# Performance work log

Measured on AMD Instinct MI355X. Metric: run time of the kernel, lower is better.

Reference implementation:

```python
import jax, jax.numpy as jnp
import numpy as np

N_GRAPHS = 1000
P = 300                 # nodes per ring graph
N = N_GRAPHS * P        # 300000 nodes
IN_DIM = 2
HID = 128
OUT_DIM = 2


def _ring_edges():
    idx = jnp.arange(N)
    g = idx // P
    pos = idx % P
    nxt = g * P + (pos + 1) % P
    src = jnp.concatenate([idx, nxt])
    dst = jnp.concatenate([nxt, idx])
    return jnp.stack([src, dst]), g


def setup_inputs() -> dict:
    key = jax.random.key(0)
    ks = jax.random.split(key, 11)
    edge_index, batch = _ring_edges()
    x = jax.random.normal(ks[0], (N, IN_DIM), jnp.float32)

    def glorot(k, fan_in, fan_out):
        lim = np.sqrt(6.0 / (fan_in + fan_out)).astype(np.float32)
        return jax.random.uniform(k, (fan_in, fan_out), jnp.float32, -lim, lim)

    return {
        "x": x,
        "edge_index": edge_index,
        "batch": batch,
        "W1": glorot(ks[1], IN_DIM, HID), "b1": jnp.zeros((HID,), jnp.float32),
        "W2": glorot(ks[2], HID, HID),    "b2": jnp.zeros((HID,), jnp.float32),
        "W3": glorot(ks[3], HID, HID),    "b3": jnp.zeros((HID,), jnp.float32),
        "fw1": glorot(ks[4], HID, HID),   "fb1": jnp.zeros((HID,), jnp.float32),
        "fw2": glorot(ks[5], HID, OUT_DIM), "fb2": jnp.zeros((OUT_DIM,), jnp.float32),
    }


def _gcn_conv(x, W, b, src, dst, norm):
    h = x @ W                              # [N, out]
    msg = h[src] * norm[:, None]           # gather + per-edge scale
    agg = jax.ops.segment_sum(msg, dst, num_segments=N)  # scatter-add
    return agg + b


def reference(x, edge_index, batch, W1, b1, W2, b2, W3, b3, fw1, fb1, fw2, fb2):
    loop = jnp.arange(N)
    src = jnp.concatenate([edge_index[0], loop])
    dst = jnp.concatenate([edge_index[1], loop])
    deg = jax.ops.segment_sum(jnp.ones_like(dst, jnp.float32), dst, num_segments=N)
    dis = jax.lax.rsqrt(deg)               # deg >= 1 due to self-loops
    norm = dis[src] * dis[dst]             # per-edge normalization

    h = jax.nn.relu(_gcn_conv(x, W1, b1, src, dst, norm))
    h = jax.nn.relu(_gcn_conv(h, W2, b2, src, dst, norm))
    h = jax.nn.relu(_gcn_conv(h, W3, b3, src, dst, norm))

    # global mean pool per graph
    sums = jax.ops.segment_sum(h, batch, num_segments=N_GRAPHS)
    cnts = jax.ops.segment_sum(jnp.ones((N,), jnp.float32), batch, num_segments=N_GRAPHS)
    pooled = sums / cnts[:, None]

    out = jax.nn.relu(pooled @ fw1 + fb1)
    out = out @ fw2 + fb2
    return out
```

## Files before the change

### kernel.cpp

```cpp
#include <hip/hip_runtime.h>
#include <hip/hip_bf16.h>
#include <stdint.h>

#define P    300
#define HID  128
#define NG   1000
#define NTL  19

typedef __attribute__((ext_vector_type(8))) short bf16x8;
typedef __attribute__((ext_vector_type(4))) short bf16x4;
typedef __attribute__((ext_vector_type(4))) float f32x4;

__device__ short g_wsw[2 * HID * HID];

__device__ __forceinline__ short f2bf(float f) {
    union { float f; uint32_t u; } v; v.f = f;
    uint32_t r = v.u + 0x7fffu + ((v.u >> 16) & 1u);
    return (short)(r >> 16);
}
__device__ __forceinline__ float bf2f(short s) {
    union { uint32_t u; float f; } v; v.u = ((uint32_t)(uint16_t)s) << 16;
    return v.f;
}
__device__ __forceinline__ uint32_t pkbf2(float a, float b) {
    union { __hip_bfloat162 h; uint32_t u; } cv;
    cv.h = __float22bfloat162_rn(float2{a, b});
    return cv.u;
}
__device__ __forceinline__ float unpk(int v, int ft) {
    return bf2f((short)(ft ? (((uint32_t)v) >> 16) : (v & 0xffff)));
}

__device__ __forceinline__ f32x4 mfma16(bf16x4 a, bf16x4 b, f32x4 c) {
#if __has_builtin(__builtin_amdgcn_mfma_f32_16x16x16bf16_1k)
    return __builtin_amdgcn_mfma_f32_16x16x16bf16_1k(a, b, c, 0, 0, 0);
#else
    asm("v_mfma_f32_16x16x16_bf16 %0, %1, %2, %0" : "+v"(c) : "v"(a), "v"(b));
    return c;
#endif
}

__global__ __launch_bounds__(256) void k_prep(const float* __restrict__ W2,
                                              const float* __restrict__ W3) {
    int b = blockIdx.x;
    const bool perm = (b < 8);
    const float* W = perm ? W2 : W3;
    short* dst = g_wsw + (perm ? 0 : HID * HID);
    int t    = (b & 7) * 256 + threadIdx.x;
    int fkey = t >> 4;
    int kc   = t & 15;
    int fsrc;
    if (perm) {
        int u = fkey >> 5, ft = (fkey >> 4) & 1, l = fkey & 15;
        fsrc = u * 32 + 2 * l + ft;
    } else fsrc = fkey;
    bf16x8 o;
    #pragma unroll
    for (int j = 0; j < 8; ++j)
        o[j] = f2bf(W[(kc * 8 + j) * HID + fsrc]);
    *(bf16x8*)&dst[(fkey * 16 + (kc ^ (fkey & 15))) * 8] = o;
}

template<int POOL>
__device__ __forceinline__ void run_pass(short* __restrict__ buf,
                                         const short* __restrict__ wbase,
                                         const float* __restrict__ bias,
                                         float* __restrict__ pool, int tid) {
    const int lane = tid & 63, wv = tid >> 6;
    const int grp = wv >> 2, w4 = wv & 3;
    const int q = lane >> 4, lm = lane & 15;
    const int ftg0 = w4 * 2;
    bf16x8 wf[2][4];
    #pragma unroll
    for (int ft = 0; ft < 2; ++ft) {
        int fkey = (ftg0 + ft) * 16 + lm;
        #pragma unroll
        for (int kk = 0; kk < 4; ++kk)
            wf[ft][kk] = *(const bf16x8*)&wbase[(fkey * 16 + ((4 * kk + q) ^ lm)) * 8];
    }
    float biaf[2];
    #pragma unroll
    for (int ft = 0; ft < 2; ++ft)
        biaf[ft] = POOL ? bias[(ftg0 + ft) * 16 + lm] : bias[w4 * 32 + 2 * lm + ft];
    const int fpair = w4 * 32 + 2 * lm;
    const int kcs = fpair >> 3, offs = fpair & 7;

    const short ONE = (short)0x3F80;
    bf16x4 Sb = {0, 0, 0, 0}, Sp = {0, 0, 0, 0}, Sn = {0, 0, 0, 0};
    #pragma unroll
    for (int j = 0; j < 4; ++j) {
        const int k = 4 * q + j;
        if (((lm & 3) == 0 && k == lm - 1) || ((lm & 3) == 3 && k == lm + 1))
            Sb[j] = ONE;
        if (lm == 0  && k == 15) Sp[j] = ONE;
        if (lm == 15 && k == 0 ) Sn[j] = ONE;
    }

    float psum[2] = {0.f, 0.f};
    float z[2];

    auto mfma_tile = [&](int t, f32x4 (&G)[2]) {
        const short* tb = buf + t * 2048;
        G[0] = f32x4{0.f, 0.f, 0.f, 0.f};
        G[1] = f32x4{0.f, 0.f, 0.f, 0.f};
        #pragma unroll
        for (int kk = 0; kk < 4; ++kk) {
            bf16x8 af = *(const bf16x8*)&tb[(lm * 16 + ((4 * kk + q) ^ lm)) * 8];
            G[0] = __builtin_amdgcn_mfma_f32_16x16x32_bf16(af, wf[0][kk], G[0], 0, 0, 0);
            G[1] = __builtin_amdgcn_mfma_f32_16x16x32_bf16(af, wf[1][kk], G[1], 0, 0, 0);
        }
    };
    auto pack = [&](const f32x4 (&G)[2], bf16x4 (&d)[2]) {
        #pragma unroll
        for (int ft = 0; ft < 2; ++ft) {
            union { bf16x4 v; uint32_t u[2]; } pk;
            pk.u[0] = pkbf2(G[ft][0], G[ft][1]);
            pk.u[1] = pkbf2(G[ft][2], G[ft][3]);
            d[ft] = pk.v;
        }
    };
    auto store_rows = [&](int T, float (&o)[2][4]) {
        #pragma unroll
        for (int i = 0; i < 4; ++i) {
            int node = T * 16 + q * 4 + i;
            *(uint32_t*)&buf[(node * 16 + (kcs ^ (node & 15))) * 8 + offs] =
                pkbf2(o[0][i], o[1][i]);
        }
    };
    auto accum = [&](float (&o)[2][4]) {
        #pragma unroll
        for (int ft = 0; ft < 2; ++ft)
            psum[ft] += o[ft][0] + o[ft][1] + o[ft][2] + o[ft][3];
    };

    auto epi = [&](const f32x4 (&E)[2], const bf16x4 (&bT)[2],
                   const bf16x4 (&bP)[2], const bf16x4 (&bN)[2],
                   int mode, float (&o)[2][4]) {
        #pragma unroll
        for (int ft = 0; ft < 2; ++ft) {
            f32x4 C = {0.f, 0.f, 0.f, 0.f};
            C = mfma16(Sb, bT[ft], C);
            if (mode != 1) C = mfma16(Sp, bP[ft], C);
            if (mode != 2) C = mfma16(Sn, bN[ft], C);
            const float s0 = E[ft][0] + E[ft][1];
            const float s2 = E[ft][2] + E[ft][3];
            float t0 = C[0] + s0;
            float t1 = s0 + E[ft][2];
            float t2 = E[ft][1] + s2;
            float t3 = s2 + C[3];
            if (mode == 1) t0 += (q == 0) ? z[ft] : 0.f;
            if (mode == 2) t3 += (q == 2) ? z[ft] : 0.f;
            float v0 = fmaf(t0, 1.f / 3.f, biaf[ft]);
            float v1 = fmaf(t1, 1.f / 3.f, biaf[ft]);
            float v2 = fmaf(t2, 1.f / 3.f, biaf[ft]);
            float v3 = fmaf(t3, 1.f / 3.f, biaf[ft]);
            o[ft][0] = v0 > 0.f ? v0 : 0.f;
            o[ft][1] = v1 > 0.f ? v1 : 0.f;
            o[ft][2] = v2 > 0.f ? v2 : 0.f;
            o[ft][3] = v3 > 0.f ? v3 : 0.f;
        }
    };

    const int base = grp ? 10 : 0;
    f32x4 Gh[2];
    bf16x4 bqM[2], bqH[2], bq9p[2];

    {
        f32x4 T[2];
        if (grp == 0) {
            mfma_tile(18, T);
            int v = __shfl((int)pkbf2(T[0][3], T[1][3]), 32 + lm, 64);
            z[0] = unpk(v, 0); z[1] = unpk(v, 1);
            mfma_tile(9, T); pack(T, bq9p);
            Gh[0] = T[0]; Gh[1] = T[1];
            bqM[0] = bq9p[0]; bqM[1] = bq9p[1];
            bqH[0] = bq9p[0]; bqH[1] = bq9p[1];
        } else {
            mfma_tile(0, T);
            int v = __shfl((int)pkbf2(T[0][0], T[1][0]), lm, 64);
            z[0] = unpk(v, 0); z[1] = unpk(v, 1);
            mfma_tile(8, T); pack(T, bqM);
            mfma_tile(9, Gh); pack(Gh, bqH);
            bq9p[0] = bqM[0]; bq9p[1] = bqM[1];
        }
    }

    for (int j = 1; j <= 5; ++j) {
        f32x4 Gc[2], Gd[2];
        bf16x4 bqC[2], bqD[2];
        if (j < 5) {
            int t0r = base + 2 * j - 2;
            mfma_tile(t0r,     Gc); pack(Gc, bqC);
            mfma_tile(t0r + 1, Gd); pack(Gd, bqD);
        } else {
            mfma_tile(base + 8, Gc); pack(Gc, bqC);
        }
        if (!POOL) __syncthreads();

        if (j == 1 && grp == 0) {
            float o[2][4];
            epi(Gc, bqC, bqC, bqD, 1, o);
            if (POOL) accum(o); else store_rows(0, o);
        } else if (j < 5) {
            int Ta = base + 2 * j - 3;
            float o[2][4];
            epi(Gh, bqH, bqM, bqC, 0, o);
            if (POOL) accum(o); else store_rows(Ta, o);
            float o2[2][4];
            epi(Gc, bqC, bqH, bqD, 0, o2);
            if (POOL) accum(o2); else store_rows(Ta + 1, o2);
        } else {
            float o[2][4];
            epi(Gh, bqH, bqM, bqC, 0, o);
            if (POOL) accum(o); else store_rows(base + 7, o);
            if (grp == 0) {
                float o2[2][4];
                epi(Gc, bqC, bqH, bq9p, 0, o2);
                if (POOL) accum(o2); else store_rows(8, o2);
            } else {
                float o2[2][4];
                epi(Gc, bqC, bqH, bqC, 2, o2);
                if (q < 3) { if (POOL) accum(o2); else store_rows(18, o2); }
            }
        }
        if (j < 5) {
            Gh[0] = Gd[0]; Gh[1] = Gd[1];
            bqM[0] = bqC[0]; bqM[1] = bqC[1];
            bqH[0] = bqD[0]; bqH[1] = bqD[1];
        }
    }

    if (POOL) {
        #pragma unroll
        for (int ft = 0; ft < 2; ++ft) {
            psum[ft] += __shfl_xor(psum[ft], 16, 64);
            psum[ft] += __shfl_xor(psum[ft], 32, 64);
        }
        if (q == 0) {
            pool[grp * 128 + ftg0 * 16 + lm]      = psum[0];
            pool[grp * 128 + ftg0 * 16 + 16 + lm] = psum[1];
        }
    }
}

__global__ __launch_bounds__(512, 2) void k_graph(
        const float* __restrict__ x,
        const float* __restrict__ W1,  const float* __restrict__ b1,
        const float* __restrict__ b2v, const float* __restrict__ b3v,
        const float* __restrict__ fw1, const float* __restrict__ fb1,
        const float* __restrict__ fw2, const float* __restrict__ fb2,
        float* __restrict__ out) {
    __shared__ __align__(16) short buf[304 * HID];
    __shared__ __align__(16) float scr[640];
    float* xs    = scr;
    float* poolv = scr;
    float* parts = scr + 256;
    float* s1    = scr + 512;

    const int g = blockIdx.x, tid = threadIdx.x;

    if (tid < 150) *(float4*)&xs[tid * 4] = *(const float4*)&x[g * 600 + tid * 4];
    __syncthreads();

    {
        const int kc1 = tid & 15;
        const int n0  = tid >> 4;
        float w1x[8], w1y[8], b1v[8];
        #pragma unroll
        for (int j = 0; j < 8; ++j) {
            w1x[j] = W1[kc1 * 8 + j];
            w1y[j] = W1[HID + kc1 * 8 + j];
            b1v[j] = b1[kc1 * 8 + j];
        }
        #pragma unroll
        for (int it = 0; it < 10; ++it) {
            int node = it * 32 + n0;
            if (node < 304) {
                uint32_t w[4] = {0u, 0u, 0u, 0u};
                if (node < P) {
                    int prev = (node == 0)     ? P - 1 : node - 1;
                    int next = (node == P - 1) ? 0     : node + 1;
                    float2 xp = *(const float2*)&xs[2 * prev];
                    float2 xc = *(const float2*)&xs[2 * node];
                    float2 xn = *(const float2*)&xs[2 * next];
                    float ax = (xp.x + xc.x + xn.x) * (1.f / 3.f);
                    float ay = (xp.y + xc.y + xn.y) * (1.f / 3.f);
                    #pragma unroll
                    for (int jj = 0; jj < 4; ++jj) {
                        float va = ax * w1x[2*jj]   + ay * w1y[2*jj]   + b1v[2*jj];
                        float vb = ax * w1x[2*jj+1] + ay * w1y[2*jj+1] + b1v[2*jj+1];
                        va = va > 0.f ? va : 0.f;
                        vb = vb > 0.f ? vb : 0.f;
                        w[jj] = pkbf2(va, vb);
                    }
                }
                *(uint4*)&buf[(node * 16 + (kc1 ^ (node & 15))) * 8] =
                    uint4{w[0], w[1], w[2], w[3]};
            }
        }
    }
    __syncthreads();

    run_pass<0>(buf, g_wsw,             b2v, poolv, tid);
    __syncthreads();
    run_pass<1>(buf, g_wsw + HID * HID, b3v, poolv, tid);
    __syncthreads();

    if (tid < 256) {
        int f = tid & 127, half = tid >> 7;
        float p = 0.f;
        const float* fw1c = fw1 + f;
        #pragma unroll 4
        for (int k = half * 64; k < half * 64 + 64; ++k)
            p += (poolv[k] + poolv[128 + k]) * fw1c[k * 128];
        parts[half * 128 + f] = p;
    }
    __syncthreads();
    if (tid < 128) {
        float o1 = fb1[tid] + (parts[tid] + parts[128 + tid]) * (1.0f / 300.0f);
        s1[tid] = o1 > 0.f ? o1 : 0.f;
    }
    __syncthreads();
    if (tid < 128) {
        int o = tid >> 6, ln = tid & 63;
        float v = s1[ln] * fw2[ln * 2 + o] + s1[ln + 64] * fw2[(ln + 64) * 2 + o];
        #pragma unroll
        for (int off = 1; off <= 32; off <<= 1)
            v += __shfl_xor(v, off, 64);
        if (ln == 0) out[g * 2 + o] = v + fb2[o];
    }
}

extern "C" void kernel_launch(void* const* d_in, const int* in_sizes, int n_in,
                              void* d_out, int out_size, void* d_ws, size_t ws_size,
                              hipStream_t stream) {
    const float* x   = (const float*)d_in[0];
    const float* W1  = (const float*)d_in[3];
    const float* b1  = (const float*)d_in[4];
    const float* W2  = (const float*)d_in[5];
    const float* b2  = (const float*)d_in[6];
    const float* W3  = (const float*)d_in[7];
    const float* b3  = (const float*)d_in[8];
    const float* fw1 = (const float*)d_in[9];
    const float* fb1 = (const float*)d_in[10];
    const float* fw2 = (const float*)d_in[11];
    const float* fb2 = (const float*)d_in[12];
    float* out = (float*)d_out;

    k_prep <<<dim3(16), dim3(256), 0, stream>>>(W2, W3);
    k_graph<<<dim3(NG), dim3(512), 0, stream>>>(x, W1, b1, b2, b3,
                                                fw1, fb1, fw2, fb2, out);
}
```

Before: 146.7 us.

## Restructure per-tile loop into single-tile rolling window with more sync steps

Replaces the 5-iteration loop that computed two MFMA tiles per step with an 11-iteration loop computing one tile per step, keeping a rolling three-tile window (M, H, C) of neighbor values. This lowers live registers (no Gd/bqD) and may raise occupancy or reduce spills. In the non-pool variant it roughly doubles the number of __syncthreads barriers and lengthens the serial chain.

```diff
diff --git a/kernel.cpp b/kernel.cpp
--- a/kernel.cpp
+++ b/kernel.cpp
@@ -161,9 +161,8 @@
         }
     };
 
-    const int base = grp ? 10 : 0;
-    f32x4 Gh[2];
-    bf16x4 bqM[2], bqH[2], bq9p[2];
+    f32x4 Gh[2], Gc[2];
+    bf16x4 bqM[2], bqH[2], bqC[2], bq9p[2];
 
     {
         f32x4 T[2];
@@ -171,62 +170,50 @@
             mfma_tile(18, T);
             int v = __shfl((int)pkbf2(T[0][3], T[1][3]), 32 + lm, 64);
             z[0] = unpk(v, 0); z[1] = unpk(v, 1);
-            mfma_tile(9, T); pack(T, bq9p);
-            Gh[0] = T[0]; Gh[1] = T[1];
-            bqM[0] = bq9p[0]; bqM[1] = bq9p[1];
-            bqH[0] = bq9p[0]; bqH[1] = bq9p[1];
         } else {
             mfma_tile(0, T);
             int v = __shfl((int)pkbf2(T[0][0], T[1][0]), lm, 64);
             z[0] = unpk(v, 0); z[1] = unpk(v, 1);
             mfma_tile(8, T); pack(T, bqM);
-            mfma_tile(9, Gh); pack(Gh, bqH);
-            bq9p[0] = bqM[0]; bq9p[1] = bqM[1];
-        }
-    }
-
-    for (int j = 1; j <= 5; ++j) {
-        f32x4 Gc[2], Gd[2];
-        bf16x4 bqC[2], bqD[2];
-        if (j < 5) {
-            int t0r = base + 2 * j - 2;
-            mfma_tile(t0r,     Gc); pack(Gc, bqC);
-            mfma_tile(t0r + 1, Gd); pack(Gd, bqD);
+            bqH[0] = bqM[0]; bqH[1] = bqM[1];
+        }
+    }
+
+    for (int s = 1; s <= 11; ++s) {
+        const bool hasRead = (s <= 10);
+        if (hasRead) {
+            int rt = grp ? (8 + s) : ((s == 1) ? 9 : s - 2);
+            mfma_tile(rt, Gc); pack(Gc, bqC);
+        }
+        if (!POOL) __syncthreads();
+
+        if (grp == 0) {
+            if (s == 1) {
+                bq9p[0] = bqC[0]; bq9p[1] = bqC[1];
+                bqH[0] = bqC[0];  bqH[1] = bqC[1];
+            } else if (s >= 3) {
+                int T = s - 3;
+                float o[2][4];
+                if (s <= 10) epi(Gh, bqH, bqM, bqC,  (T == 0) ? 1 : 0, o);
+                else         epi(Gh, bqH, bqM, bq9p, 0, o);
+                if (POOL) accum(o); else store_rows(T, o);
+            }
         } else {
-            mfma_tile(base + 8, Gc); pack(Gc, bqC);
-        }
-        if (!POOL) __syncthreads();
-
-        if (j == 1 && grp == 0) {
-            float o[2][4];
-            epi(Gc, bqC, bqC, bqD, 1, o);
-            if (POOL) accum(o); else store_rows(0, o);
-        } else if (j < 5) {
-            int Ta = base + 2 * j - 3;
-            float o[2][4];
-            epi(Gh, bqH, bqM, bqC, 0, o);
-            if (POOL) accum(o); else store_rows(Ta, o);
-            float o2[2][4];
-            epi(Gc, bqC, bqH, bqD, 0, o2);
-            if (POOL) accum(o2); else store_rows(Ta + 1, o2);
-        } else {
-            float o[2][4];
-            epi(Gh, bqH, bqM, bqC, 0, o);
-            if (POOL) accum(o); else store_rows(base + 7, o);
-            if (grp == 0) {
-                float o2[2][4];
-                epi(Gc, bqC, bqH, bq9p, 0, o2);
-                if (POOL) accum(o2); else store_rows(8, o2);
-            } else {
-                float o2[2][4];
-                epi(Gc, bqC, bqH, bqC, 2, o2);
-                if (q < 3) { if (POOL) accum(o2); else store_rows(18, o2); }
+            if (s >= 2) {
+                float o[2][4];
+                if (s <= 10) {
+                    epi(Gh, bqH, bqM, bqC, 0, o);
+                    if (POOL) accum(o); else store_rows(7 + s, o);
+                } else {
+                    epi(Gh, bqH, bqM, bqH, 2, o);
+                    if (q < 3) { if (POOL) accum(o); else store_rows(18, o); }
+                }
             }
         }
-        if (j < 5) {
-            Gh[0] = Gd[0]; Gh[1] = Gd[1];
-            bqM[0] = bqC[0]; bqM[1] = bqC[1];
-            bqH[0] = bqD[0]; bqH[1] = bqD[1];
+        if (hasRead && !(grp == 0 && s == 1)) {
+            Gh[0] = Gc[0];  Gh[1] = Gc[1];
+            bqM[0] = bqH[0]; bqM[1] = bqH[1];
+            bqH[0] = bqC[0]; bqH[1] = bqC[1];
         }
     }
 
```

After: 129.9 us. 11.5% less time.
